# Performance work log

Hardware: AMD Instinct MI355X
Metric: run time of the kernel (lower is better)

Reference implementation:

```python
import jax, jax.numpy as jnp
import numpy as np

N_NODES = 65536
N_FEAT = 64
N_EDGES = 1048576
N_GRAPHS = 16
LP_ITERS = 30


def setup_inputs() -> dict:
    key = jax.random.key(0)
    k1, k2, k3 = jax.random.split(key, 3)
    x = jax.random.normal(k1, (N_NODES, N_FEAT), dtype=jnp.float32)
    edge_index = jax.random.randint(k2, (2, N_EDGES), 0, N_NODES, dtype=jnp.int32)
    batch = jnp.sort(jax.random.randint(k3, (N_NODES,), 0, N_GRAPHS, dtype=jnp.int32))
    v2 = jnp.full((1,), 3.5, dtype=jnp.float32)  # learnable affinity scale param
    return {"x": x, "edge_index": edge_index, "batch": batch, "v2": v2}


def _lp_clustering(row, col, aff, n_nodes, n_iters):
    """Label propagation: each node adopts the neighbor label with max summed affinity."""
    E = row.shape[0]
    aff = jax.lax.stop_gradient(aff)  # clustering is discrete, no grad path

    def body(_, labels):
        lab_c = labels[col]                                    # neighbor labels per edge
        order = jnp.lexsort((lab_c, row))                      # sort by (row, neighbor-label)
        r_s, l_s, w_s = row[order], lab_c[order], aff[order]
        new_grp = jnp.concatenate([jnp.ones((1,), bool),
                                   (r_s[1:] != r_s[:-1]) | (l_s[1:] != l_s[:-1])])
        gid = jnp.cumsum(new_grp) - 1                          # dense (row,label) group ids
        gsum = jax.ops.segment_sum(w_s, gid, num_segments=E)   # affinity mass per group
        gcnt = jax.ops.segment_sum(jnp.ones_like(w_s), gid, num_segments=E)
        valid = gcnt > 0
        g_row = jnp.where(valid, jax.ops.segment_max(r_s, gid, num_segments=E), 0)
        g_lab = jnp.where(valid, jax.ops.segment_max(l_s, gid, num_segments=E), n_nodes)
        node_max = jax.ops.segment_max(jnp.where(valid, gsum, -jnp.inf), g_row,
                                       num_segments=n_nodes)
        win = valid & (gsum == node_max[g_row])
        # smallest winning label == torch argmax first-hit tie-break
        return jax.ops.segment_min(jnp.where(win, g_lab, n_nodes), g_row,
                                   num_segments=n_nodes)

    labels0 = jnp.arange(n_nodes, dtype=row.dtype)
    return jax.lax.fori_loop(0, n_iters, body, labels0)


def _forward(x, edge_index, batch, v2):
    n = x.shape[0]
    loops = jnp.arange(n, dtype=edge_index.dtype)
    ei = jnp.concatenate([edge_index, jnp.stack([loops, loops])], axis=1)  # add_self_loops
    row, col = ei[0], ei[1]

    # P2-style affinities: log_aff = -v2 * ||x_i - x_j||^2 ; forward exponentiates
    sqdist = jnp.sum((x[row] - x[col]) ** 2, axis=1)  # [E]
    losses = jnp.mean(sqdist)
    aff = jnp.exp(-v2[0] * sqdist)

    node_labels = _lp_clustering(row, col, aff, n, LP_ITERS)

    # unique(return_inverse): dense relabel of surviving cluster ids (sorted order)
    present = jnp.zeros((n,), jnp.int32).at[node_labels].set(1)
    cluster_labels = (jnp.cumsum(present) - 1)[node_labels]

    # max_pool_x: scatter-max node features into clusters (padded to n rows)
    cx = jax.ops.segment_max(x, cluster_labels, num_segments=n)
    cb = jax.ops.segment_max(batch, cluster_labels, num_segments=n)
    nonempty = jax.ops.segment_sum(jnp.ones((n,), jnp.int32), cluster_labels,
                                   num_segments=n) > 0
    cx = jnp.where(nonempty[:, None], cx, 0.0)
    cb = jnp.where(nonempty, cb, -1)

    # coalesce(cluster_labels[edge_index]): sort + dedupe, duplicates padded with -1
    mr, mc = cluster_labels[row], cluster_labels[col]
    order = jnp.lexsort((mc, mr))
    mr_s, mc_s = mr[order], mc[order]
    dup = jnp.concatenate([jnp.zeros((1,), bool),
                           (mr_s[1:] == mr_s[:-1]) & (mc_s[1:] == mc_s[:-1])])
    cei = jnp.stack([jnp.where(dup, -1, mr_s), jnp.where(dup, -1, mc_s)])

    return cx, cei, cb, cluster_labels, losses


def reference(x, edge_index, batch, v2):
    return _forward(x, edge_index, batch, v2)
```

## Files before the change

### kernel.cpp

```cpp
#include <hip/hip_runtime.h>
#include <hip/hip_fp16.h>
#include <hip/hip_cooperative_groups.h>

namespace cg = cooperative_groups;

#define DI __device__ __forceinline__

constexpr int NN   = 65536;
constexpr int NF   = 64;
constexpr int E0c  = 1048576;
constexpr int ET   = E0c + NN;
constexpr int LPITERS = 30;
constexpr int KPOS = 16;
constexpr int MSCH = 4096;
constexpr int NCHK = ET / MSCH;
constexpr int SCAP = 8192;
constexpr int CAP0 = 6144;
constexpr int BPB  = CAP0 / 64;
constexpr int NPART2 = 256 * BPB;

constexpr int O_CX   = 0;
constexpr int O_CEI0 = NN * NF;
constexpr int O_CEI1 = O_CEI0 + ET;
constexpr int O_CB   = O_CEI0 + 2 * ET;
constexpr int O_CL   = O_CB + NN;
constexpr int O_LOSS = O_CL + NN;

constexpr int W_CHG   = 0;
constexpr int W_NCLUS = 32;
constexpr int W_H1    = 64;
constexpr int W_GC0   = W_H1 + 256;
constexpr int W_GC1   = W_GC0 + 256;
constexpr int W_SCP   = 832;
constexpr int W_SCO   = W_SCP + 256;
constexpr int W_PART  = W_SCO + 256;
constexpr int W_PCNT  = W_PART + NPART2;
constexpr int W_PCOL  = W_PCNT + NN;
constexpr int W_PW    = W_PCOL + NN*KPOS;
constexpr int W_L0    = W_PW + NN*KPOS;
constexpr int W_L1    = W_L0 + NN;
constexpr int W_PRES  = W_L1 + NN;
constexpr int W_PSUM  = W_PRES + NN;
constexpr int W_CLU   = W_PSUM + NN;
constexpr int W_CBA   = W_CLU + NN;
constexpr int W_K0    = W_CBA + NN;
constexpr int W_K1    = W_K0 + 256*CAP0;

DI void edge_rc(const int* ei, int e, int& r, int& c) {
  if (e < E0c) { r = ei[e]; c = ei[E0c + e]; }
  else         { r = e - E0c; c = r; }
}

DI unsigned fenc(float f) {
  unsigned u = __float_as_uint(f);
  return (u & 0x80000000u) ? ~u : (u | 0x80000000u);
}
DI float fdec(unsigned u) {
  u = (u & 0x80000000u) ? (u & 0x7fffffffu) : ~u;
  return __uint_as_float(u);
}

DI int lp_step(int r, int d, int c0, int c1, float q0, float q1,
               const int* __restrict__ pcol, const float* __restrict__ pw,
               const int* __restrict__ lin) {
  int bl = NN;
  if (d == 1) {
    bl = lin[c0];
  } else if (d == 2) {
    int l0 = lin[c0], l1 = lin[c1];
    if (l0 == l1) bl = l0;
    else if (q1 > q0 || (q1 == q0 && l1 < l0)) bl = l1;
    else bl = l0;
  } else if (d > 2) {
    float best = 0.f;
    for (int i = 0; i < d; ++i) {
      int li = lin[pcol[r * KPOS + i]];
      bool dup = false;
      for (int j = 0; j < i; ++j)
        if (lin[pcol[r * KPOS + j]] == li) { dup = true; break; }
      if (dup) continue;
      float sum = 0.f;
      for (int j = i; j < d; ++j)
        if (lin[pcol[r * KPOS + j]] == li) sum += pw[r * KPOS + j];
      if (sum > best || (sum == best && li < bl)) { best = sum; bl = li; }
    }
  }
  return bl;
}


__global__ __launch_bounds__(256) void init_small(int* ws) {
  for (int i = threadIdx.x; i < 832; i += 256) ws[i] = 0;
}

__global__ __launch_bounds__(256) void emultisplit(const int* __restrict__ ei,
                                                   int* __restrict__ gcur0,
                                                   unsigned* __restrict__ K0,
                                                   int* __restrict__ pcnt,
                                                   int* __restrict__ L0,
                                                   const float2* __restrict__ x2,
                                                   unsigned* __restrict__ xh) {
  __shared__ unsigned skey[MSCH];
  __shared__ unsigned short binid[MSCH];
  __shared__ int hl[256], ss[256], hs[256], hc[256], gb[256];
  int t = threadIdx.x;
  if (blockIdx.x < 256) {
    int rr = blockIdx.x * 256 + t;
    pcnt[rr] = 0;
    L0[rr] = rr;
  }
  for (int i = blockIdx.x * 256 + t; i < NN * NF / 2; i += NCHK * 256) {
    float2 f = x2[i];
    __half2 h = __floats2half2_rn(f.x, f.y);
    xh[i] = *reinterpret_cast<unsigned*>(&h);
  }
  hl[t] = 0; __syncthreads();
  int base = blockIdx.x * MSCH;
  unsigned mykey[MSCH / 256];
  #pragma unroll
  for (int k = 0; k < MSCH / 256; ++k) {
    int e = base + k * 256 + t;
    int r, c; edge_rc(ei, e, r, c);
    unsigned key = ((unsigned)r << 16) | (unsigned)c;
    mykey[k] = key;
    atomicAdd(&hl[key >> 24], 1);
  }
  __syncthreads();
  int v = hl[t];
  ss[t] = v; __syncthreads();
  for (int off = 1; off < 256; off <<= 1) {
    int u = (t >= off) ? ss[t - off] : 0;
    __syncthreads();
    ss[t] += u;
    __syncthreads();
  }
  int excl = ss[t] - v;
  hs[t] = excl;
  hc[t] = excl;
  gb[t] = t * CAP0 + ((v > 0) ? atomicAdd(&gcur0[t], v) : 0);
  for (int j = excl; j < excl + v; ++j) binid[j] = (unsigned short)t;
  __syncthreads();
  #pragma unroll
  for (int k = 0; k < MSCH / 256; ++k) {
    int b = mykey[k] >> 24;
    int slot = atomicAdd(&hc[b], 1);
    skey[slot] = mykey[k];
  }
  __syncthreads();
  for (int i = t; i < MSCH; i += 256) {
    int b = binid[i];
    int pos = gb[b] + (i - hs[b]);
    if (pos < (b + 1) * CAP0) K0[pos] = skey[i];
  }
}

__global__ __launch_bounds__(256) void edge_pos2(const unsigned* __restrict__ xh,
                                                 const unsigned* __restrict__ K0,
                                                 const int* __restrict__ gcur0,
                                                 const float* __restrict__ v2,
                                                 float* __restrict__ part,
                                                 int* __restrict__ pcnt,
                                                 int* __restrict__ pcol,
                                                 float* __restrict__ pw) {
  __shared__ float ls[32];
  int t = threadIdx.x, grp = t >> 3, lane = t & 7;
  int bkt = blockIdx.x / BPB;
  int off = (blockIdx.x % BPB) * 64;
  int cnt = gcur0[bkt];
  if (off >= cnt) {
    if (t == 0) part[blockIdx.x] = 0.f;
    return;
  }
  float w = v2[0];
  unsigned kk[2]; bool act[2];
  uint4 A[2], B[2];
  #pragma unroll
  for (int q = 0; q < 2; ++q) {
    int j = off + grp * 2 + q;
    act[q] = (j < cnt);
    kk[q] = K0[bkt * CAP0 + (act[q] ? j : 0)];
  }
  #pragma unroll
  for (int q = 0; q < 2; ++q) {
    int r = kk[q] >> 16, c = kk[q] & 0xFFFF;
    A[q] = ((const uint4*)(xh + (size_t)r * 32))[lane];
    B[q] = ((const uint4*)(xh + (size_t)c * 32))[lane];
  }
  __builtin_amdgcn_sched_barrier(0);
  float lsum = 0.f;
  #pragma unroll
  for (int q = 0; q < 2; ++q) {
    const __half2* ah = reinterpret_cast<const __half2*>(&A[q]);
    const __half2* bh = reinterpret_cast<const __half2*>(&B[q]);
    __half2 d0 = __hsub2(ah[0], bh[0]);
    __half2 acc = __hmul2(d0, d0);
    __half2 d1 = __hsub2(ah[1], bh[1]); acc = __hfma2(d1, d1, acc);
    __half2 d2 = __hsub2(ah[2], bh[2]); acc = __hfma2(d2, d2, acc);
    __half2 d3 = __hsub2(ah[3], bh[3]); acc = __hfma2(d3, d3, acc);
    float s = __low2float(acc) + __high2float(acc);
    s += __shfl_xor(s, 1, 8);
    s += __shfl_xor(s, 2, 8);
    s += __shfl_xor(s, 4, 8);
    if (lane == 0 && act[q]) {
      int r = kk[q] >> 16, c = kk[q] & 0xFFFF;
      if (r == c) s = 0.f;
      lsum += s;
      float aff = expf(-w * s);
      if (aff > 0.f) {
        int slot = atomicAdd(&pcnt[r], 1);
        if (slot < KPOS) { pcol[r * KPOS + slot] = c; pw[r * KPOS + slot] = aff; }
      }
    }
  }
  if (lane == 0) ls[grp] = lsum;
  __syncthreads();
  if (t == 0) {
    float s = 0.f;
    #pragma unroll
    for (int k = 0; k < 32; ++k) s += ls[k];
    part[blockIdx.x] = s;
  }
}

__global__ __launch_bounds__(256) void lp_iter0(const int* __restrict__ pcnt,
                                                const int* __restrict__ pcol,
                                                const float* __restrict__ pw,
                                                const int* __restrict__ L0,
                                                int* __restrict__ L1,
                                                int* __restrict__ chg,
                                                const float* __restrict__ part,
                                                float* __restrict__ out_loss) {
  __shared__ float smf[256];
  int t = threadIdx.x;
  int r = blockIdx.x * 256 + t;
  int d = pcnt[r];
  if (d > KPOS) d = KPOS;
  int c0 = 0, c1 = 0; float q0 = 0.f, q1 = 0.f;
  if (d >= 1) { c0 = pcol[r * KPOS];     q0 = pw[r * KPOS]; }
  if (d >= 2) { c1 = pcol[r * KPOS + 1]; q1 = pw[r * KPOS + 1]; }
  int bl = lp_step(r, d, c0, c1, q0, q1, pcol, pw, L0);
  L1[r] = bl;
  if (bl != L0[r]) atomicOr(&chg[0], 1);
  if (blockIdx.x == 0) {
    float s = 0.f;
    for (int i = t; i < NPART2; i += 256) s += part[i];
    smf[t] = s; __syncthreads();
    for (int off = 128; off; off >>= 1) {
      if (t < off) smf[t] += smf[t + off];
      __syncthreads();
    }
    if (t == 0) out_loss[0] = smf[0] / (float)ET;
  }
}

__global__ __launch_bounds__(256) void general_tail(
    const int* __restrict__ pcnt, const int* __restrict__ pcol,
    const float* __restrict__ pw, int* __restrict__ L0, int* __restrict__ L1,
    int* __restrict__ chg, int* __restrict__ pres, int* __restrict__ psum,
    int* __restrict__ clu, float* __restrict__ out_cl, int* __restrict__ cba,
    unsigned* __restrict__ cxacc, const float* __restrict__ x,
    const int* __restrict__ batch, int* __restrict__ nclus_g,
    int* __restrict__ scp, int* __restrict__ sco, int* __restrict__ h1,
    const int* __restrict__ gcur0, int* __restrict__ gcur1,
    const unsigned* __restrict__ K0, unsigned* __restrict__ K1,
    float* __restrict__ out_cb) {
  if (chg[0] == 0) return;
  __shared__ int sm[256], hl[256], bases[256];
  __shared__ int sbc;
  cg::grid_group grid = cg::this_grid();
  int t = threadIdx.x, b = blockIdx.x;
  int r = b * 256 + t;
  pres[r] = 0;
  cba[r] = -1;
  {
    uint4 z = make_uint4(0u, 0u, 0u, 0u);
    uint4* p = (uint4*)(cxacc + ((size_t)r << 6));
    #pragma unroll
    for (int q = 0; q < 16; ++q) p[q] = z;
  }
  int mylab = L1[r];
  int d = pcnt[r]; if (d > KPOS) d = KPOS;
  int c0 = 0, c1 = 0; float q0 = 0.f, q1 = 0.f;
  if (d >= 1) { c0 = pcol[r * KPOS];     q0 = pw[r * KPOS]; }
  if (d >= 2) { c1 = pcol[r * KPOS + 1]; q1 = pw[r * KPOS + 1]; }
  for (int it = 1; it < LPITERS; ++it) {
    const int* lin = (it & 1) ? L1 : L0;
    int* lout = (it & 1) ? L0 : L1;
    int bl = lp_step(r, d, c0, c1, q0, q1, pcol, pw, lin);
    lout[r] = bl;
    if (bl != mylab) atomicOr(&chg[it], 1);
    mylab = bl;
    grid.sync();
    if (t == 0) sbc = *(volatile int*)&chg[it];
    __syncthreads();
    if (sbc == 0) break;
  }
  L0[r] = mylab;
  grid.sync();
  pres[mylab] = 1;
  grid.sync();
  int v = pres[r];
  sm[t] = v; __syncthreads();
  for (int off = 1; off < 256; off <<= 1) {
    int u = (t >= off) ? sm[t - off] : 0;
    __syncthreads();
    sm[t] += u;
    __syncthreads();
  }
  int lexcl = sm[t] - v;
  if (t == 255) scp[b] = sm[255];
  grid.sync();
  if (b == 0) {
    int p = scp[t];
    sm[t] = p; __syncthreads();
    for (int off = 1; off < 256; off <<= 1) {
      int u = (t >= off) ? sm[t - off] : 0;
      __syncthreads();
      sm[t] += u;
      __syncthreads();
    }
    sco[t] = sm[t] - p;
    if (t == 255) nclus_g[0] = sm[255];
  }
  grid.sync();
  psum[r] = lexcl + sco[b];
  grid.sync();
  int cr = psum[mylab];
  clu[r] = cr;
  out_cl[r] = (float)cr;
  grid.sync();
  for (int f = 0; f < 64; ++f)
    atomicMax(&cxacc[((size_t)cr << 6) + f], fenc(x[((size_t)r << 6) + f]));
  atomicMax(&cba[cr], batch[r]);
  grid.sync();
  int ncl = nclus_g[0];
  for (int f = 0; f < 64; ++f) {
    unsigned u = cxacc[((size_t)r << 6) + f];
    ((float*)cxacc)[((size_t)r << 6) + f] = (r < ncl) ? fdec(u) : 0.f;
  }
  out_cb[r] = (float)cba[r];
  hl[t] = 0; __syncthreads();
  int cnt = gcur0[b];
  for (int i = t; i < cnt; i += 256) {
    unsigned k = K0[b * CAP0 + i];
    atomicAdd(&hl[((unsigned)clu[k >> 16]) >> 8], 1);
  }
  __syncthreads();
  if (hl[t]) atomicAdd(&h1[t], hl[t]);
  grid.sync();
  int hv = h1[t];
  sm[t] = hv; __syncthreads();
  for (int off = 1; off < 256; off <<= 1) {
    int u = (t >= off) ? sm[t - off] : 0;
    __syncthreads();
    sm[t] += u;
    __syncthreads();
  }
  bases[t] = sm[t] - hv;
  __syncthreads();
  for (int i = t; i < cnt; i += 256) {
    unsigned k = K0[b * CAP0 + i];
    unsigned k1 = ((unsigned)clu[k >> 16] << 16) | (unsigned)clu[k & 0xFFFF];
    int b1 = k1 >> 24;
    int pos = bases[b1] + atomicAdd(&gcur1[b1], 1);
    K1[pos] = k1;
  }
}

__global__ __launch_bounds__(512) void sortwrite_fast(
    const unsigned* __restrict__ K0, const int* __restrict__ gcur0,
    const int* __restrict__ chg, const float4* __restrict__ x4,
    const int* __restrict__ batch, float4* __restrict__ out_cx4,
    float* __restrict__ out_cl, float* __restrict__ out_cb,
    float* __restrict__ o0, float* __restrict__ o1) {
  if (chg[0] != 0) return;
  __shared__ unsigned sk[CAP0];
  __shared__ int hl[256], ss[256], sbs[257], cur[256], sh[2];
  int t = threadIdx.x;
  int b = blockIdx.x >> 2, spl = blockIdx.x & 3;
  {
    int base4 = blockIdx.x * 1024;
    for (int i = t; i < 1024; i += 512) out_cx4[base4 + i] = x4[base4 + i];
    int rbase = blockIdx.x * 64;
    for (int i = t; i < 64; i += 512) {
      out_cl[rbase + i] = (float)(rbase + i);
      out_cb[rbase + i] = (float)batch[rbase + i];
    }
  }
  int cntb = gcur0[b];
  if (cntb > CAP0) cntb = CAP0;
  if (t < 256) ss[t] = gcur0[t];
  __syncthreads();
  for (int off = 1; off < 256; off <<= 1) {
    int u = (t < 256 && t >= off) ? ss[t - off] : 0;
    __syncthreads();
    if (t < 256) ss[t] += u;
    __syncthreads();
  }
  if (t == 0) sh[0] = ss[b] - gcur0[b];
  if (t < 256) hl[t] = 0;
  __syncthreads();
  for (int i = t; i < cntb; i += 512)
    atomicAdd(&hl[(K0[b * CAP0 + i] >> 16) & 0xFF], 1);
  __syncthreads();
  if (t < 256) ss[t] = hl[t];
  __syncthreads();
  for (int off = 1; off < 256; off <<= 1) {
    int u = (t < 256 && t >= off) ? ss[t - off] : 0;
    __syncthreads();
    if (t < 256) ss[t] += u;
    __syncthreads();
  }
  if (t < 256) { sbs[t] = ss[t] - hl[t]; cur[t] = ss[t] - hl[t]; }
  if (t == 255) sbs[256] = cntb;
  __syncthreads();
  int sout_b = sh[0];
  int sb0 = spl * 64, sb1 = sb0 + 64;
  int mybase = sbs[sb0], myend = sbs[sb1];
  if (myend <= mybase) return;
  for (int i = t; i < cntb; i += 512) {
    unsigned k = K0[b * CAP0 + i];
    int sb = (k >> 16) & 0xFF;
    if (sb >= sb0 && sb < sb1) {
      int slot = atomicAdd(&cur[sb], 1);
      sk[slot - mybase] = k;
    }
  }
  __syncthreads();
  int wave = t >> 6, lane = t & 63;
  for (int sb = sb0 + wave; sb < sb1; sb += 8) {
    int s0 = sbs[sb] - mybase, s1 = sbs[sb + 1] - mybase, dd = s1 - s0;
    if (dd <= 1) continue;
    if (dd <= 64) {
      unsigned k = (lane < dd) ? sk[s0 + lane] : 0xFFFFFFFFu;
      int P = (dd <= 16) ? 16 : ((dd <= 32) ? 32 : 64);
      for (int size = 2; size <= P; size <<= 1) {
        bool upAll = (size == P);
        for (int stride = size >> 1; stride > 0; stride >>= 1) {
          unsigned o = __shfl_xor(k, stride, 64);
          bool up = upAll || ((lane & size) == 0);
          bool takeMin = (((lane & stride) == 0) == up);
          unsigned mn = k < o ? k : o, mx = k < o ? o : k;
          k = takeMin ? mn : mx;
        }
      }
      if (lane < dd) sk[s0 + lane] = k;
    } else if (lane == 0) {
      for (int i = s0 + 1; i < s1; ++i) {
        unsigned k = sk[i];
        int j = i - 1;
        while (j >= s0 && sk[j] > k) { sk[j + 1] = sk[j]; --j; }
        sk[j + 1] = k;
      }
    }
  }
  __syncthreads();
  int mycnt = myend - mybase;
  for (int i = t; i < mycnt; i += 512) {
    unsigned k = sk[i];
    bool dup = (i > 0) && (sk[i - 1] == k);
    int gp = sout_b + mybase + i;
    o0[gp] = dup ? -1.f : (float)(k >> 16);
    o1[gp] = dup ? -1.f : (float)(k & 0xffffu);
  }
}

__global__ __launch_bounds__(512) void sortwrite_general(
    unsigned* __restrict__ K1, const int* __restrict__ h1,
    const int* __restrict__ chg, float* __restrict__ o0,
    float* __restrict__ o1) {
  if (chg[0] == 0) return;
  __shared__ unsigned sk[SCAP];
  __shared__ int hl[256], ss[256], sbs[257], cur[256], sh[2];
  int t = threadIdx.x, b = blockIdx.x;
  if (t < 256) ss[t] = h1[t];
  __syncthreads();
  for (int off = 1; off < 256; off <<= 1) {
    int u = (t < 256 && t >= off) ? ss[t - off] : 0;
    __syncthreads();
    if (t < 256) ss[t] += u;
    __syncthreads();
  }
  if (t == 0) { sh[0] = ss[b] - h1[b]; sh[1] = h1[b]; }
  __syncthreads();
  int sout = sh[0], d = sh[1];
  if (d <= 0) return;
  unsigned* kp = K1 + sout;
  if (d <= SCAP) {
    if (t < 256) hl[t] = 0;
    __syncthreads();
    for (int i = t; i < d; i += 512)
      atomicAdd(&hl[(kp[i] >> 16) & 0xFF], 1);
    __syncthreads();
    if (t < 256) ss[t] = hl[t];
    __syncthreads();
    for (int off = 1; off < 256; off <<= 1) {
      int u = (t < 256 && t >= off) ? ss[t - off] : 0;
      __syncthreads();
      if (t < 256) ss[t] += u;
      __syncthreads();
    }
    if (t < 256) { sbs[t] = ss[t] - hl[t]; cur[t] = ss[t] - hl[t]; }
    if (t == 255) sbs[256] = d;
    __syncthreads();
    for (int i = t; i < d; i += 512) {
      unsigned k = kp[i];
      int slot = atomicAdd(&cur[(k >> 16) & 0xFF], 1);
      sk[slot] = k;
    }
    __syncthreads();
    int wave = t >> 6, lane = t & 63;
    for (int sb = wave; sb < 256; sb += 8) {
      int s0 = sbs[sb], s1 = sbs[sb + 1], dd = s1 - s0;
      if (dd <= 1) continue;
      if (dd <= 64) {
        unsigned k = (lane < dd) ? sk[s0 + lane] : 0xFFFFFFFFu;
        #pragma unroll
        for (int size = 2; size <= 64; size <<= 1) {
          #pragma unroll
          for (int stride = size >> 1; stride > 0; stride >>= 1) {
            unsigned o = __shfl_xor(k, stride, 64);
            bool takeMin = (((lane & stride) == 0) == ((lane & size) == 0));
            unsigned mn = k < o ? k : o, mx = k < o ? o : k;
            k = takeMin ? mn : mx;
          }
        }
        if (lane < dd) sk[s0 + lane] = k;
      } else if (lane == 0) {
        for (int i = s0 + 1; i < s1; ++i) {
          unsigned k = sk[i];
          int j = i - 1;
          while (j >= s0 && sk[j] > k) { sk[j + 1] = sk[j]; --j; }
          sk[j + 1] = k;
        }
      }
    }
    __syncthreads();
    for (int i = t; i < d; i += 512) {
      unsigned k = sk[i];
      bool dup = (i > 0) && (sk[i - 1] == k);
      o0[sout + i] = dup ? -1.f : (float)(k >> 16);
      o1[sout + i] = dup ? -1.f : (float)(k & 0xffffu);
    }
  } else {
    if (t == 0) {
      for (int i = 1; i < d; ++i) {
        unsigned k = kp[i];
        int j = i - 1;
        while (j >= 0 && kp[j] > k) { kp[j + 1] = kp[j]; --j; }
        kp[j + 1] = k;
      }
    }
    __syncthreads();
    for (int i = t; i < d; i += 512) {
      unsigned k = kp[i];
      bool dup = (i > 0) && (kp[i - 1] == k);
      o0[sout + i] = dup ? -1.f : (float)(k >> 16);
      o1[sout + i] = dup ? -1.f : (float)(k & 0xffffu);
    }
  }
}


extern "C" void kernel_launch(void* const* d_in, const int* in_sizes, int n_in,
                              void* d_out, int out_size, void* d_ws, size_t ws_size,
                              hipStream_t stream) {
  const float* x   = (const float*)d_in[0];
  const int* ei    = (const int*)d_in[1];
  const int* batch = (const int*)d_in[2];
  const float* v2  = (const float*)d_in[3];
  float* out = (float*)d_out;
  int* ws = (int*)d_ws;
  unsigned* cxacc = (unsigned*)(out + O_CX);
  unsigned* xh = cxacc;

  init_small<<<1, 256, 0, stream>>>(ws);

  emultisplit<<<NCHK, 256, 0, stream>>>(ei, ws + W_GC0, (unsigned*)(ws + W_K0),
                                        ws + W_PCNT, ws + W_L0,
                                        (const float2*)x, xh);

  edge_pos2<<<NPART2, 256, 0, stream>>>(xh, (const unsigned*)(ws + W_K0),
                                        ws + W_GC0, v2, (float*)(ws + W_PART),
                                        ws + W_PCNT, ws + W_PCOL, (float*)(ws + W_PW));

  lp_iter0<<<NN / 256, 256, 0, stream>>>(ws + W_PCNT, ws + W_PCOL,
                                         (const float*)(ws + W_PW),
                                         ws + W_L0, ws + W_L1, ws + W_CHG,
                                         (const float*)(ws + W_PART), out + O_LOSS);

  {
    const int* pcnt = ws + W_PCNT;
    const int* pcol = ws + W_PCOL;
    const float* pw = (const float*)(ws + W_PW);
    int* L0 = ws + W_L0;
    int* L1 = ws + W_L1;
    int* chg = ws + W_CHG;
    int* pres = ws + W_PRES;
    int* psum = ws + W_PSUM;
    int* clu = ws + W_CLU;
    float* out_cl = out + O_CL;
    int* cba = ws + W_CBA;
    unsigned* cxa = cxacc;
    const float* x_ = x;
    const int* batch_ = batch;
    int* nclus_g = ws + W_NCLUS;
    int* scp = ws + W_SCP;
    int* sco = ws + W_SCO;
    int* h1 = ws + W_H1;
    const int* gcur0 = ws + W_GC0;
    int* gcur1 = ws + W_GC1;
    const unsigned* K0 = (const unsigned*)(ws + W_K0);
    unsigned* K1 = (unsigned*)(ws + W_K1);
    float* out_cb = out + O_CB;
    void* args[] = { (void*)&pcnt, (void*)&pcol, (void*)&pw,
                     (void*)&L0, (void*)&L1, (void*)&chg, (void*)&pres,
                     (void*)&psum, (void*)&clu, (void*)&out_cl, (void*)&cba,
                     (void*)&cxa, (void*)&x_, (void*)&batch_, (void*)&nclus_g,
                     (void*)&scp, (void*)&sco, (void*)&h1, (void*)&gcur0,
                     (void*)&gcur1, (void*)&K0, (void*)&K1, (void*)&out_cb };
    hipLaunchCooperativeKernel((const void*)general_tail, dim3(NN / 256),
                               dim3(256), args, 0, stream);
  }

  sortwrite_fast<<<1024, 512, 0, stream>>>((const unsigned*)(ws + W_K0),
                                           ws + W_GC0, ws + W_CHG,
                                           (const float4*)x, batch,
                                           (float4*)(out + O_CX), out + O_CL,
                                           out + O_CB, out + O_CEI0,
                                           out + O_CEI1);

  sortwrite_general<<<256, 512, 0, stream>>>((unsigned*)(ws + W_K1), ws + W_H1,
                                             ws + W_CHG, out + O_CEI0,
                                             out + O_CEI1);
}
```

Before: 151.7 us.

## Split feature copy out of sort kernel and widen per-block edge work

The edge distance kernel now processes four edges per 8-lane group (128 per block) instead of two, halving the block count and raising memory-level parallelism per thread. The fast-path sort kernel no longer splits each bucket across four blocks that each rescanned the whole bucket; one 1024-thread block now handles a full bucket. The x/cluster/batch output copy moves to a separate simple kernel. The changes trade fewer redundant bucket scans for lower block count and higher register use in the edge kernel.

```diff
diff --git a/kernel.cpp b/kernel.cpp
--- a/kernel.cpp
+++ b/kernel.cpp
@@ -16,7 +16,8 @@
 constexpr int NCHK = ET / MSCH;
 constexpr int SCAP = 8192;
 constexpr int CAP0 = 6144;
-constexpr int BPB  = CAP0 / 64;
+constexpr int EPB  = 128;
+constexpr int BPB  = CAP0 / EPB;
 constexpr int NPART2 = 256 * BPB;
 
 constexpr int O_CX   = 0;
@@ -165,23 +166,23 @@
   __shared__ float ls[32];
   int t = threadIdx.x, grp = t >> 3, lane = t & 7;
   int bkt = blockIdx.x / BPB;
-  int off = (blockIdx.x % BPB) * 64;
+  int off = (blockIdx.x % BPB) * EPB;
   int cnt = gcur0[bkt];
   if (off >= cnt) {
     if (t == 0) part[blockIdx.x] = 0.f;
     return;
   }
   float w = v2[0];
-  unsigned kk[2]; bool act[2];
-  uint4 A[2], B[2];
+  unsigned kk[4]; bool act[4];
+  uint4 A[4], B[4];
   #pragma unroll
-  for (int q = 0; q < 2; ++q) {
-    int j = off + grp * 2 + q;
+  for (int q = 0; q < 4; ++q) {
+    int j = off + grp * 4 + q;
     act[q] = (j < cnt);
     kk[q] = K0[bkt * CAP0 + (act[q] ? j : 0)];
   }
   #pragma unroll
-  for (int q = 0; q < 2; ++q) {
+  for (int q = 0; q < 4; ++q) {
     int r = kk[q] >> 16, c = kk[q] & 0xFFFF;
     A[q] = ((const uint4*)(xh + (size_t)r * 32))[lane];
     B[q] = ((const uint4*)(xh + (size_t)c * 32))[lane];
@@ -189,7 +190,7 @@
   __builtin_amdgcn_sched_barrier(0);
   float lsum = 0.f;
   #pragma unroll
-  for (int q = 0; q < 2; ++q) {
+  for (int q = 0; q < 4; ++q) {
     const __half2* ah = reinterpret_cast<const __half2*>(&A[q]);
     const __half2* bh = reinterpret_cast<const __half2*>(&B[q]);
     __half2 d0 = __hsub2(ah[0], bh[0]);
@@ -367,26 +368,30 @@
   }
 }
 
-__global__ __launch_bounds__(512) void sortwrite_fast(
+__global__ __launch_bounds__(256) void fast_copy(const int* __restrict__ chg,
+                                                 const float4* __restrict__ x4,
+                                                 const int* __restrict__ batch,
+                                                 float4* __restrict__ out_cx4,
+                                                 float* __restrict__ out_cl,
+                                                 float* __restrict__ out_cb) {
+  if (chg[0] != 0) return;
+  int i = blockIdx.x * 256 + threadIdx.x;
+  out_cx4[i] = x4[i];
+  out_cx4[i + 524288] = x4[i + 524288];
+  if (i < NN) {
+    out_cl[i] = (float)i;
+    out_cb[i] = (float)batch[i];
+  }
+}
+
+__global__ __launch_bounds__(1024) void sortwrite_fast(
     const unsigned* __restrict__ K0, const int* __restrict__ gcur0,
-    const int* __restrict__ chg, const float4* __restrict__ x4,
-    const int* __restrict__ batch, float4* __restrict__ out_cx4,
-    float* __restrict__ out_cl, float* __restrict__ out_cb,
-    float* __restrict__ o0, float* __restrict__ o1) {
+    const int* __restrict__ chg, float* __restrict__ o0,
+    float* __restrict__ o1) {
   if (chg[0] != 0) return;
   __shared__ unsigned sk[CAP0];
-  __shared__ int hl[256], ss[256], sbs[257], cur[256], sh[2];
-  int t = threadIdx.x;
-  int b = blockIdx.x >> 2, spl = blockIdx.x & 3;
-  {
-    int base4 = blockIdx.x * 1024;
-    for (int i = t; i < 1024; i += 512) out_cx4[base4 + i] = x4[base4 + i];
-    int rbase = blockIdx.x * 64;
-    for (int i = t; i < 64; i += 512) {
-      out_cl[rbase + i] = (float)(rbase + i);
-      out_cb[rbase + i] = (float)batch[rbase + i];
-    }
-  }
+  __shared__ int hl[256], ss[256], sbs[257], cur[256], sh[1];
+  int t = threadIdx.x, b = blockIdx.x;
   int cntb = gcur0[b];
   if (cntb > CAP0) cntb = CAP0;
   if (t < 256) ss[t] = gcur0[t];
@@ -400,7 +405,7 @@
   if (t == 0) sh[0] = ss[b] - gcur0[b];
   if (t < 256) hl[t] = 0;
   __syncthreads();
-  for (int i = t; i < cntb; i += 512)
+  for (int i = t; i < cntb; i += 1024)
     atomicAdd(&hl[(K0[b * CAP0 + i] >> 16) & 0xFF], 1);
   __syncthreads();
   if (t < 256) ss[t] = hl[t];
@@ -414,22 +419,15 @@
   if (t < 256) { sbs[t] = ss[t] - hl[t]; cur[t] = ss[t] - hl[t]; }
   if (t == 255) sbs[256] = cntb;
   __syncthreads();
-  int sout_b = sh[0];
-  int sb0 = spl * 64, sb1 = sb0 + 64;
-  int mybase = sbs[sb0], myend = sbs[sb1];
-  if (myend <= mybase) return;
-  for (int i = t; i < cntb; i += 512) {
+  for (int i = t; i < cntb; i += 1024) {
     unsigned k = K0[b * CAP0 + i];
-    int sb = (k >> 16) & 0xFF;
-    if (sb >= sb0 && sb < sb1) {
-      int slot = atomicAdd(&cur[sb], 1);
-      sk[slot - mybase] = k;
-    }
+    int slot = atomicAdd(&cur[(k >> 16) & 0xFF], 1);
+    sk[slot] = k;
   }
   __syncthreads();
   int wave = t >> 6, lane = t & 63;
-  for (int sb = sb0 + wave; sb < sb1; sb += 8) {
-    int s0 = sbs[sb] - mybase, s1 = sbs[sb + 1] - mybase, dd = s1 - s0;
+  for (int sb = wave; sb < 256; sb += 16) {
+    int s0 = sbs[sb], s1 = sbs[sb + 1], dd = s1 - s0;
     if (dd <= 1) continue;
     if (dd <= 64) {
       unsigned k = (lane < dd) ? sk[s0 + lane] : 0xFFFFFFFFu;
@@ -455,13 +453,12 @@
     }
   }
   __syncthreads();
-  int mycnt = myend - mybase;
-  for (int i = t; i < mycnt; i += 512) {
+  int sout = sh[0];
+  for (int i = t; i < cntb; i += 1024) {
     unsigned k = sk[i];
     bool dup = (i > 0) && (sk[i - 1] == k);
-    int gp = sout_b + mybase + i;
-    o0[gp] = dup ? -1.f : (float)(k >> 16);
-    o1[gp] = dup ? -1.f : (float)(k & 0xffffu);
+    o0[sout + i] = dup ? -1.f : (float)(k >> 16);
+    o1[sout + i] = dup ? -1.f : (float)(k & 0xffffu);
   }
 }
 
@@ -623,12 +620,13 @@
                                dim3(256), args, 0, stream);
   }
 
-  sortwrite_fast<<<1024, 512, 0, stream>>>((const unsigned*)(ws + W_K0),
+  fast_copy<<<2048, 256, 0, stream>>>(ws + W_CHG, (const float4*)x, batch,
+                                      (float4*)(out + O_CX), out + O_CL,
+                                      out + O_CB);
+
+  sortwrite_fast<<<256, 1024, 0, stream>>>((const unsigned*)(ws + W_K0),
                                            ws + W_GC0, ws + W_CHG,
-                                           (const float4*)x, batch,
-                                           (float4*)(out + O_CX), out + O_CL,
-                                           out + O_CB, out + O_CEI0,
-                                           out + O_CEI1);
+                                           out + O_CEI0, out + O_CEI1);
 
   sortwrite_general<<<256, 512, 0, stream>>>((unsigned*)(ws + W_K1), ws + W_H1,
                                              ws + W_CHG, out + O_CEI0,
```

New measurement: 143.8 us. -5.2%, faster.
